# Kernel optimization log

Hardware: AMD Instinct MI355X
Metric: run time of the kernel (lower is better)

## Reference

```python
import jax, jax.numpy as jnp
import numpy as np

EPS = 1e-12  # matches torch.nn.functional.normalize eps


def _normalize(x):
    n = jnp.sqrt(jnp.sum(x * x, axis=-1, keepdims=True))
    return x / jnp.maximum(n, EPS)


def setup_inputs() -> dict:
    key = jax.random.key(0)
    k1, k2, k3 = jax.random.split(key, 3)
    B, C, D = 1024, 32768, 512
    embeddings = jax.random.normal(k1, (B, D), dtype=jnp.float32)
    proxies = jax.random.normal(k2, (C, D), dtype=jnp.float32) / 8.0
    labels = jax.random.randint(k3, (B,), 0, C, dtype=jnp.int64)
    return {"embeddings": embeddings, "proxies": proxies, "labels": labels}


def reference(embeddings, proxies, labels):
    # batch: [B, D], P: [C, D], both scaled to norm 3
    batch = 3.0 * _normalize(embeddings)
    P = 3.0 * _normalize(proxies)

    # Squared euclidean distances to ALL proxies via the expansion
    # ||b - p||^2 = ||b||^2 + ||p||^2 - 2 b.p  -> [B, C]
    b_sq = jnp.sum(batch * batch, axis=-1, keepdims=True)      # [B, 1]
    p_sq = jnp.sum(P * P, axis=-1)                             # [C]
    dist = b_sq + p_sq[None, :] - 2.0 * (batch @ P.T)          # [B, C]

    B = batch.shape[0]
    rows = jnp.arange(B)
    pos_dist = dist[rows, labels]                              # [B]

    # logsumexp over negatives: mask out the positive class per row
    neg_scores = jnp.where(
        jnp.arange(dist.shape[1])[None, :] == labels[:, None],
        -jnp.inf,
        -dist,
    )
    neg_lse = jax.nn.logsumexp(neg_scores, axis=1)             # [B]

    return jnp.mean(pos_dist + neg_lse)
```

## Files before the change

kernel.cpp:

```cpp
#include <hip/hip_runtime.h>
#include <hip/hip_fp8.h>
#include <stdint.h>

#define D_DIM 512
#define B_ROWS 1024
#define C_ROWS 32768
#define NBLK (C_ROWS / 128)

typedef __attribute__((ext_vector_type(4))) float floatx4;
typedef __attribute__((ext_vector_type(2))) long longx2;

#define GLOBAL_AS __attribute__((address_space(1)))
#define LDS_AS __attribute__((address_space(3)))

__device__ inline void async_copy16(const unsigned char* g, unsigned char* l) {
    __builtin_amdgcn_global_load_lds((const GLOBAL_AS void*)g, (LDS_AS void*)l, 16, 0, 0);
}

__device__ inline unsigned char f2fp8(float x) {
    __hip_fp8_e4m3 t(x);
    return t.__x;
}
__device__ inline float fp8tof(unsigned char v) {
    __hip_fp8_e4m3 t;
    t.__x = v;
    return (float)t;
}


__global__ void norm_rows_kernel(const float* __restrict__ prox,
                                 const float* __restrict__ emb,
                                 unsigned char* __restrict__ Pq,
                                 unsigned char* __restrict__ Aq,
                                 float* __restrict__ acc,
                                 unsigned* __restrict__ ticket) {
    if (blockIdx.x == 0 && threadIdx.x == 0) { *acc = 0.f; *ticket = 0u; }
    const int wid = threadIdx.x >> 6;
    const int lane = threadIdx.x & 63;
    int row = blockIdx.x * 4 + wid;
    const float* src;
    unsigned char* dst;
    if (row < C_ROWS) {
        src = prox; dst = Pq;
    } else {
        row -= C_ROWS;
        src = emb; dst = Aq;
    }

    const float4* p = (const float4*)(src + (size_t)row * D_DIM + lane * 8);
    float4 v0 = p[0];
    float4 v1 = p[1];
    float ss = v0.x * v0.x + v0.y * v0.y + v0.z * v0.z + v0.w * v0.w +
               v1.x * v1.x + v1.y * v1.y + v1.z * v1.z + v1.w * v1.w;
#pragma unroll
    for (int off = 1; off < 64; off <<= 1) ss += __shfl_xor(ss, off);
    const float s = 3.0f * rsqrtf(ss);

    unsigned char q[8];
    q[0] = f2fp8(v0.x * s); q[1] = f2fp8(v0.y * s);
    q[2] = f2fp8(v0.z * s); q[3] = f2fp8(v0.w * s);
    q[4] = f2fp8(v1.x * s); q[5] = f2fp8(v1.y * s);
    q[6] = f2fp8(v1.z * s); q[7] = f2fp8(v1.w * s);
    uint2 packed;
    packed.x = (unsigned)q[0] | ((unsigned)q[1] << 8) |
               ((unsigned)q[2] << 16) | ((unsigned)q[3] << 24);
    packed.y = (unsigned)q[4] | ((unsigned)q[5] << 8) |
               ((unsigned)q[6] << 16) | ((unsigned)q[7] << 24);

    const size_t u = ((size_t)(row >> 4) * 8 + (lane >> 3)) * 64 +
                     (lane & 3) * 16 + (row & 15);
    *(uint2*)(dst + u * 16 + ((lane >> 2) & 1) * 8) = packed;
}

__global__ void __launch_bounds__(256, 4)
gemm_lse_kernel(const unsigned char* __restrict__ Aq,
                const unsigned char* __restrict__ Bq,
                float* __restrict__ part) {
    __shared__ unsigned char sA[16384];
    __shared__ unsigned char sB[16384];
    __shared__ float red[128];

    const int tid = threadIdx.x;
    const int wid = tid >> 6;
    const int lane = tid & 63;
    const int n0t = blockIdx.x * 8;
    const int m0t = blockIdx.y * 8;

    if (tid < 128) red[tid] = 0.f;

    const int wmt = (wid >> 1) * 4;
    const int wnt = (wid & 1) * 4;
    const int wm = wmt * 16;
    const int fr = lane & 15;
    const int quad = lane >> 4;

    floatx4 acc[4][4];
    const floatx4 zero = {0.f, 0.f, 0.f, 0.f};
#pragma unroll
    for (int i = 0; i < 4; ++i)
#pragma unroll
        for (int j = 0; j < 4; ++j) acc[i][j] = zero;

    for (int c = 0; c < 4; ++c) {
#pragma unroll
        for (int j = 0; j < 4; ++j) {
            const int tl = wid * 2 + (j >> 1);
            const int sp = j & 1;
            const size_t goA = (((size_t)(m0t + tl) * 8 + 2 * c + sp) * 64 + lane) * 16;
            const size_t goB = (((size_t)(n0t + tl) * 8 + 2 * c + sp) * 64 + lane) * 16;
            const int lo = ((tl * 2 + sp) * 64 + lane) * 16;
            async_copy16(Aq + goA, &sA[lo]);
            async_copy16(Bq + goB, &sB[lo]);
        }
        __syncthreads();

#pragma unroll
        for (int p = 0; p < 2; ++p) {
            longx2 a2[4], b2[4];
#pragma unroll
            for (int t = 0; t < 4; ++t) {
                a2[t] = *(const longx2*)&sA[(((wmt + t) * 2 + p) * 64 + lane) * 16];
                b2[t] = *(const longx2*)&sB[(((wnt + t) * 2 + p) * 64 + lane) * 16];
            }
#pragma unroll
            for (int ti = 0; ti < 4; ++ti)
#pragma unroll
                for (int tj = 0; tj < 4; ++tj)
                    acc[ti][tj] = __builtin_amdgcn_mfma_f32_16x16x32_fp8_fp8(
                        a2[ti][0], b2[tj][0], acc[ti][tj], 0, 0, 0);
#pragma unroll
            for (int ti = 0; ti < 4; ++ti)
#pragma unroll
                for (int tj = 0; tj < 4; ++tj)
                    acc[ti][tj] = __builtin_amdgcn_mfma_f32_16x16x32_fp8_fp8(
                        a2[ti][1], b2[tj][1], acc[ti][tj], 0, 0, 0);
        }
        __syncthreads();
    }

#pragma unroll
    for (int ti = 0; ti < 4; ++ti) {
        float rs[4] = {0.f, 0.f, 0.f, 0.f};
#pragma unroll
        for (int tj = 0; tj < 4; ++tj)
#pragma unroll
            for (int r = 0; r < 4; ++r)
                rs[r] += __expf(2.0f * acc[ti][tj][r]);
#pragma unroll
        for (int r = 0; r < 4; ++r) {
            rs[r] += __shfl_xor(rs[r], 1);
            rs[r] += __shfl_xor(rs[r], 2);
            rs[r] += __shfl_xor(rs[r], 4);
            rs[r] += __shfl_xor(rs[r], 8);
        }
        if (fr == 0) {
#pragma unroll
            for (int r = 0; r < 4; ++r)
                atomicAdd(&red[wm + ti * 16 + quad * 4 + r], rs[r]);
        }
    }
    __syncthreads();
    if (tid < 128)
        part[(size_t)blockIdx.x * B_ROWS + m0t * 16 + tid] = red[tid];
}

__global__ void finalize_kernel(const float* __restrict__ part,
                                const unsigned char* __restrict__ Aq,
                                const unsigned char* __restrict__ Pq,
                                const int* __restrict__ labels,
                                float* __restrict__ acc,
                                unsigned* __restrict__ ticket,
                                float* __restrict__ out) {
    __shared__ float r4s[4];
    const int tid = threadIdx.x;
    const int wid = tid >> 6;
    const int lane = tid & 63;
    const int b = blockIdx.x * 4 + wid;

    float s = 0.f;
#pragma unroll
    for (int k = 0; k < 4; ++k)
        s += part[(size_t)(lane * 4 + k) * B_ROWS + b];

    const int l = labels[b];
    const size_t ua_u = ((size_t)(b >> 4) * 8 + (lane >> 3)) * 64 +
                        (lane & 3) * 16 + (b & 15);
    const size_t ub_u = ((size_t)(l >> 4) * 8 + (lane >> 3)) * 64 +
                        (lane & 3) * 16 + (l & 15);
    uint2 ua = *(const uint2*)(Aq + ua_u * 16 + ((lane >> 2) & 1) * 8);
    uint2 ub = *(const uint2*)(Pq + ub_u * 16 + ((lane >> 2) & 1) * 8);
    const unsigned char* au = (const unsigned char*)&ua;
    const unsigned char* bu = (const unsigned char*)&ub;
    float d = 0.f;
#pragma unroll
    for (int j = 0; j < 8; ++j) d += fp8tof(au[j]) * fp8tof(bu[j]);
#pragma unroll
    for (int off = 1; off < 64; off <<= 1) {
        s += __shfl_xor(s, off);
        d += __shfl_xor(d, off);
    }

    if (lane == 0) {
        float p2 = 2.0f * d;
        r4s[wid] = logf(s - __expf(p2)) - p2;
    }
    __syncthreads();
    if (tid == 0) {
        float bl = r4s[0] + r4s[1] + r4s[2] + r4s[3];
        atomicAdd(acc, bl);
        __threadfence();
        unsigned t = atomicAdd(ticket, 1u);
        if (t == 255u) {
            float total = atomicAdd(acc, 0.f);
            out[0] = total / (float)B_ROWS;
        }
    }
}

extern "C" void kernel_launch(void* const* d_in, const int* in_sizes, int n_in,
                              void* d_out, int out_size, void* d_ws, size_t ws_size,
                              hipStream_t stream) {
    const float* emb = (const float*)d_in[0];
    const float* prox = (const float*)d_in[1];
    const int* labels = (const int*)d_in[2];
    float* out = (float*)d_out;

    char* ws = (char*)d_ws;
    unsigned char* Pq = (unsigned char*)ws;
    unsigned char* Aq = Pq + (size_t)C_ROWS * D_DIM;
    float* part = (float*)(Aq + (size_t)B_ROWS * D_DIM);
    float* acc = part + (size_t)NBLK * B_ROWS;
    unsigned* ticket = (unsigned*)(acc + 1);

    norm_rows_kernel<<<(C_ROWS + B_ROWS) / 4, 256, 0, stream>>>(
        prox, emb, Pq, Aq, acc, ticket);
    gemm_lse_kernel<<<dim3(NBLK, B_ROWS / 128), 256, 0, stream>>>(Aq, Pq, part);
    finalize_kernel<<<B_ROWS / 4, 256, 0, stream>>>(
        part, Aq, Pq, labels, acc, ticket, out);
}
```

Before: 139.4 us.

## Switch FP8 GEMM to 16x16x128 scaled MFMA with matching K-packed layout

Replaces the 16x16x32 fp8 MFMA with the gfx950 scaled 16x16x128 f8f6f4 MFMA (unit scales), issuing a quarter as many matrix instructions per K chunk. The quantized operand layout written by the normalization kernel and read by the finalize kernel is rearranged so each lane can load its 32 fp8 bytes for the wider K step with two 16-byte LDS reads. The launch-bounds occupancy hint is also lowered from 4 to 3 waves per SIMD. This risks register pressure from the wider operands and depends on the new layout exactly matching the instruction's operand mapping.

Result: no change. 136.9 us (-1.8%).

```diff
diff --git a/kernel.cpp b/kernel.cpp
--- a/kernel.cpp
+++ b/kernel.cpp
@@ -8,7 +8,8 @@
 #define NBLK (C_ROWS / 128)
 
 typedef __attribute__((ext_vector_type(4))) float floatx4;
-typedef __attribute__((ext_vector_type(2))) long longx2;
+typedef __attribute__((ext_vector_type(4))) int intx4;
+typedef __attribute__((ext_vector_type(8))) int intx8;
 
 #define GLOBAL_AS __attribute__((address_space(1)))
 #define LDS_AS __attribute__((address_space(3)))
@@ -67,17 +68,18 @@
     packed.y = (unsigned)q[4] | ((unsigned)q[5] << 8) |
                ((unsigned)q[6] << 16) | ((unsigned)q[7] << 24);
 
-    const size_t u = ((size_t)(row >> 4) * 8 + (lane >> 3)) * 64 +
-                     (lane & 3) * 16 + (row & 15);
-    *(uint2*)(dst + u * 16 + ((lane >> 2) & 1) * 8) = packed;
-}
-
-__global__ void __launch_bounds__(256, 4)
+    const size_t addr = (size_t)(row >> 4) * 8192 + (lane >> 4) * 2048 +
+                        ((lane >> 1) & 1) * 1024 + ((lane >> 2) & 3) * 256 +
+                        (row & 15) * 16 + (lane & 1) * 8;
+    *(uint2*)(dst + addr) = packed;
+}
+
+__global__ void __launch_bounds__(256, 3)
 gemm_lse_kernel(const unsigned char* __restrict__ Aq,
                 const unsigned char* __restrict__ Bq,
                 float* __restrict__ part) {
-    __shared__ unsigned char sA[16384];
-    __shared__ unsigned char sB[16384];
+    __shared__ __align__(16) unsigned char sA[16384];
+    __shared__ __align__(16) unsigned char sB[16384];
     __shared__ float red[128];
 
     const int tid = threadIdx.x;
@@ -105,36 +107,35 @@
 #pragma unroll
         for (int j = 0; j < 4; ++j) {
             const int tl = wid * 2 + (j >> 1);
-            const int sp = j & 1;
-            const size_t goA = (((size_t)(m0t + tl) * 8 + 2 * c + sp) * 64 + lane) * 16;
-            const size_t goB = (((size_t)(n0t + tl) * 8 + 2 * c + sp) * 64 + lane) * 16;
-            const int lo = ((tl * 2 + sp) * 64 + lane) * 16;
-            async_copy16(Aq + goA, &sA[lo]);
-            async_copy16(Bq + goB, &sB[lo]);
+            const int half = j & 1;
+            const size_t goA = (size_t)(m0t + tl) * 8192 + c * 2048 + half * 1024;
+            const size_t goB = (size_t)(n0t + tl) * 8192 + c * 2048 + half * 1024;
+            const int lo = tl * 2048 + half * 1024 + lane * 16;
+            async_copy16(Aq + goA + lane * 16, &sA[lo]);
+            async_copy16(Bq + goB + lane * 16, &sB[lo]);
         }
         __syncthreads();
 
-#pragma unroll
-        for (int p = 0; p < 2; ++p) {
-            longx2 a2[4], b2[4];
-#pragma unroll
-            for (int t = 0; t < 4; ++t) {
-                a2[t] = *(const longx2*)&sA[(((wmt + t) * 2 + p) * 64 + lane) * 16];
-                b2[t] = *(const longx2*)&sB[(((wnt + t) * 2 + p) * 64 + lane) * 16];
-            }
-#pragma unroll
-            for (int ti = 0; ti < 4; ++ti)
-#pragma unroll
-                for (int tj = 0; tj < 4; ++tj)
-                    acc[ti][tj] = __builtin_amdgcn_mfma_f32_16x16x32_fp8_fp8(
-                        a2[ti][0], b2[tj][0], acc[ti][tj], 0, 0, 0);
-#pragma unroll
-            for (int ti = 0; ti < 4; ++ti)
-#pragma unroll
-                for (int tj = 0; tj < 4; ++tj)
-                    acc[ti][tj] = __builtin_amdgcn_mfma_f32_16x16x32_fp8_fp8(
-                        a2[ti][1], b2[tj][1], acc[ti][tj], 0, 0, 0);
-        }
+        intx8 a8[4], b8[4];
+#pragma unroll
+        for (int t = 0; t < 4; ++t) {
+            const int oa = (wmt + t) * 2048 + lane * 16;
+            const int ob = (wnt + t) * 2048 + lane * 16;
+            intx4 alo = *(const intx4*)&sA[oa];
+            intx4 ahi = *(const intx4*)&sA[oa + 1024];
+            intx4 blo = *(const intx4*)&sB[ob];
+            intx4 bhi = *(const intx4*)&sB[ob + 1024];
+            a8[t] = __builtin_shufflevector(alo, ahi, 0, 1, 2, 3, 4, 5, 6, 7);
+            b8[t] = __builtin_shufflevector(blo, bhi, 0, 1, 2, 3, 4, 5, 6, 7);
+        }
+#pragma unroll
+        for (int ti = 0; ti < 4; ++ti)
+#pragma unroll
+            for (int tj = 0; tj < 4; ++tj)
+                acc[ti][tj] = __builtin_amdgcn_mfma_scale_f32_16x16x128_f8f6f4(
+                    a8[ti], b8[tj], acc[ti][tj],
+                    0 , 0 ,
+                    0, 0x7F , 0, 0x7F );
         __syncthreads();
     }
 
@@ -183,12 +184,14 @@
         s += part[(size_t)(lane * 4 + k) * B_ROWS + b];
 
     const int l = labels[b];
-    const size_t ua_u = ((size_t)(b >> 4) * 8 + (lane >> 3)) * 64 +
-                        (lane & 3) * 16 + (b & 15);
-    const size_t ub_u = ((size_t)(l >> 4) * 8 + (lane >> 3)) * 64 +
-                        (lane & 3) * 16 + (l & 15);
-    uint2 ua = *(const uint2*)(Aq + ua_u * 16 + ((lane >> 2) & 1) * 8);
-    uint2 ub = *(const uint2*)(Pq + ub_u * 16 + ((lane >> 2) & 1) * 8);
+    const size_t ua_addr = (size_t)(b >> 4) * 8192 + (lane >> 4) * 2048 +
+                           ((lane >> 1) & 1) * 1024 + ((lane >> 2) & 3) * 256 +
+                           (b & 15) * 16 + (lane & 1) * 8;
+    const size_t ub_addr = (size_t)(l >> 4) * 8192 + (lane >> 4) * 2048 +
+                           ((lane >> 1) & 1) * 1024 + ((lane >> 2) & 3) * 256 +
+                           (l & 15) * 16 + (lane & 1) * 8;
+    uint2 ua = *(const uint2*)(Aq + ua_addr);
+    uint2 ub = *(const uint2*)(Pq + ub_addr);
     const unsigned char* au = (const unsigned char*)&ua;
     const unsigned char* bu = (const unsigned char*)&ub;
     float d = 0.f;
```
